# Optimization experiments

Measured on AMD Instinct MI355X. Metric: run time of the kernel, lower is better.

## Reference

```python
import jax, jax.numpy as jnp
import numpy as np

K, T, RHO, V, TH, EH, S, B = 50, 50, 300, 20000, 800, 200, 10, 256
DELTA = 0.005
LOG_DELTA = float(np.log(DELTA))
EPS = 1e-6


def setup_inputs() -> dict:
    key = jax.random.key(0)
    ks = jax.random.split(key, 32)
    f32 = jnp.float32
    rn = lambda i, shp, s=0.02: jax.random.normal(ks[i], shp, f32) * s
    inp = {
        "unique_tokens": jax.random.randint(ks[0], (100,), 0, V),
        "bows": jax.random.uniform(ks[1], (B, V), f32),
        "normalized_bows": jax.random.uniform(ks[2], (B, V), f32),
        "times": jax.random.randint(ks[3], (B,), 0, T),
        "sources": jax.random.randint(ks[4], (B,), 0, S),
        "rnn_inp": jax.random.normal(ks[5], (S, T, V), f32),
        "num_docs": 100000,
        # learned parameters
        "mu_q_alpha": rn(6, (K, T, RHO), 1.0),
        "logsigma_q_alpha": rn(7, (K, T, RHO), 0.1),
        "rho_W": rn(8, (V, RHO)),                 # Linear(rho_size -> vocab, no bias)
        "W1": rn(9, (TH, V + K)), "b1": jnp.zeros((TH,), f32),
        "W2": rn(10, (TH, TH)), "b2": jnp.zeros((TH,), f32),
        "mu_th_W": rn(11, (K, TH)), "mu_th_b": jnp.zeros((K,), f32),
        "ls_th_W": rn(12, (K, TH)), "ls_th_b": jnp.zeros((K,), f32),
        "eta_map_W": rn(13, (EH, V)), "eta_map_b": jnp.zeros((EH,), f32),
        "lstm_Wih": rn(14, (4 * EH, EH)), "lstm_Whh": rn(15, (4 * EH, EH)),
        "lstm_bih": jnp.zeros((4 * EH,), f32), "lstm_bhh": jnp.zeros((4 * EH,), f32),
        "mu_eta_W": rn(16, (K, EH + K)), "mu_eta_b": jnp.zeros((K,), f32),
        "ls_eta_W": rn(17, (K, EH + K)), "ls_eta_b": jnp.zeros((K,), f32),
        "cls_W": rn(18, (S, K)), "cls_b": jnp.zeros((S,), f32),
    }
    return inp


def _lstm(x_seq, Wih, Whh, bih, bhh):
    # x_seq: [T, S, EH]; torch gate order i,f,g,o
    def step(carry, x):
        h, c = carry
        z = x @ Wih.T + bih + h @ Whh.T + bhh
        i, f, g, o = jnp.split(z, 4, axis=-1)
        c = jax.nn.sigmoid(f) * c + jax.nn.sigmoid(i) * jnp.tanh(g)
        h = jax.nn.sigmoid(o) * jnp.tanh(c)
        return (h, c), h
    h0 = jnp.zeros((x_seq.shape[1], Whh.shape[1]), x_seq.dtype)
    _, out = jax.lax.scan(step, (h0, h0), x_seq)
    return out  # [T, S, EH]


def reference(unique_tokens, bows, normalized_bows, times, sources, rnn_inp, num_docs,
              mu_q_alpha, logsigma_q_alpha, rho_W, W1, b1, W2, b2,
              mu_th_W, mu_th_b, ls_th_W, ls_th_b, eta_map_W, eta_map_b,
              lstm_Wih, lstm_Whh, lstm_bih, lstm_bhh,
              mu_eta_W, mu_eta_b, ls_eta_W, ls_eta_b, cls_W, cls_b):
    # eval-mode semantics: reparameterize returns mu, dropout off
    bsz = bows.shape[0]
    coeff = num_docs / bsz

    # ---- alpha: eval-mode alphas_t == mu_q_alpha[:, t, :]; KL vectorized ----
    mu_a, ls_a = mu_q_alpha, logsigma_q_alpha  # [K, T, RHO]
    kl_a0 = 0.5 * jnp.sum((jnp.exp(ls_a[:, 0]) + mu_a[:, 0] ** 2) / (1.0 + EPS) - 1.0 - ls_a[:, 0])
    diff = mu_a[:, 1:] - mu_a[:, :-1]
    kl_at = 0.5 * jnp.sum((jnp.exp(ls_a[:, 1:]) + diff ** 2) / (DELTA + EPS) - 1.0 + LOG_DELTA - ls_a[:, 1:])
    kl_alpha = kl_a0 + kl_at
    alphas = jnp.transpose(mu_a, (1, 0, 2))  # [T, K, RHO]

    # ---- eta: LSTM over time (vmapped over sources as batch), then recurrence ----
    mapped = jnp.einsum('stv,hv->sth', rnn_inp, eta_map_W) + eta_map_b  # [S, T, EH]
    lstm_out = _lstm(jnp.transpose(mapped, (1, 0, 2)), lstm_Wih, lstm_Whh, lstm_bih, lstm_bhh)  # [T, S, EH]

    inp0 = jnp.concatenate([lstm_out[0], jnp.zeros((S, K), lstm_out.dtype)], axis=-1)
    mu0 = inp0 @ mu_eta_W.T + mu_eta_b
    ls0 = inp0 @ ls_eta_W.T + ls_eta_b  # no clipping at t=0 in original
    kl0 = 0.5 * jnp.sum((jnp.exp(ls0) + mu0 ** 2) / (1.0 + EPS) - 1.0 - ls0)

    def eta_step(carry, out_t):
        eta_prev, kl = carry
        inp_t = jnp.concatenate([out_t, eta_prev], axis=-1)
        mu_t = inp_t @ mu_eta_W.T + mu_eta_b
        ls_t = jnp.clip(inp_t @ ls_eta_W.T + ls_eta_b, -10.0, 10.0)
        kl_t = 0.5 * jnp.sum((jnp.exp(ls_t) + (mu_t - eta_prev) ** 2) / (DELTA + EPS) - 1.0 + LOG_DELTA - ls_t)
        return (mu_t, kl + kl_t), mu_t
    (_, kl_rest), etas_rest = jax.lax.scan(eta_step, (mu0, jnp.float32(0.0)), lstm_out[1:])
    etas = jnp.transpose(jnp.concatenate([mu0[None], etas_rest], axis=0), (1, 0, 2))  # [S, T, K]
    kl_eta = kl0 + kl_rest

    # ---- theta ----
    eta_std = etas[sources, times]  # [B, K]
    h = jax.nn.relu(jnp.concatenate([normalized_bows, eta_std], axis=1) @ W1.T + b1)
    h = jax.nn.relu(h @ W2.T + b2)
    mu_t = h @ mu_th_W.T + mu_th_b
    ls_t = jnp.clip(h @ ls_th_W.T + ls_th_b, -10.0, 10.0)
    theta = jax.nn.softmax(mu_t, axis=-1)
    kl_theta = (0.5 * jnp.sum((jnp.exp(ls_t) + (mu_t - eta_std) ** 2) / (1.0 + EPS) - 1.0 - ls_t)) * coeff

    # ---- beta and NLL ----
    logit = jnp.einsum('tkr,vr->tkv', alphas, rho_W)
    beta = jax.nn.softmax(logit, axis=-1)        # [T, K, V]
    beta_d = beta[times]                         # [B, K, V]
    loglik = jnp.log(jnp.einsum('bk,bkv->bv', theta, beta_d))
    nll = -jnp.sum(loglik * bows) * coeff

    # ---- source prediction loss (sum-reduced cross entropy) ----
    logits = theta @ cls_W.T + cls_b
    logp = jax.nn.log_softmax(logits, axis=-1)
    pred_loss = -jnp.sum(jnp.take_along_axis(logp, sources[:, None], axis=1)) * coeff

    nelbo = nll + kl_alpha + kl_eta + kl_theta + pred_loss
    return (nelbo, nll, kl_alpha, kl_eta, kl_theta, pred_loss)
```

## Files before the change

kernel.cpp:

```cpp
#include <hip/hip_runtime.h>

typedef unsigned int u32;
typedef unsigned short ushort_t;

#define NTOP 50
#define NT_T 50
#define NRHO 300
#define NVOC 20000
#define NTH 800
#define NEH 200
#define NSRC 10
#define NBAT 256

#define OFF_SCAL     0
#define OFF_MAPPED   16
#define OFF_HPRE     100016
#define OFF_H2       304816
#define OFF_Z        509616
#define OFF_DOCCNT   512120
#define OFF_DOCLIST  512176
#define MEMSET_BYTES ((size_t)524976 * 4)
#define OFF_XW       524976
#define OFF_BIAS2    924976
#define OFF_ETAS     925776
#define OFF_WCOEF    950776
#define OFF_W1E      963576
#define OFF_WHH_H    1003576
#define OFF_ETAWH    1083576
#define OFF_H1B      1096376
#define OFF_MAPB     1198776
#define OFF_WIHB     1256120
#define OFF_W2B      1356472
#define OFF_ALPHAB   1714872
#define OFF_RHOB     2124472
#define OFF_NBB      5339832
#define OFF_W1B      7899832
#define OFF_RNNB     16859832
#define OFF_EMWB     21979832
#define OFF_LOGITH   7899832

typedef _Float16 h2v __attribute__((ext_vector_type(2)));
typedef __bf16 bf16x8 __attribute__((ext_vector_type(8)));
typedef float f32x4 __attribute__((ext_vector_type(4)));

#define REP25(M) M(0) M(1) M(2) M(3) M(4) M(5) M(6) M(7) M(8) M(9) M(10) M(11) M(12) \
                 M(13) M(14) M(15) M(16) M(17) M(18) M(19) M(20) M(21) M(22) M(23) M(24)
#define REP7(M) M(0) M(1) M(2) M(3) M(4) M(5) M(6)

__device__ inline float dot2u(u32 a, u32 b, float c){
  h2v ha = __builtin_bit_cast(h2v, a), hb = __builtin_bit_cast(h2v, b);
#if __has_builtin(__builtin_amdgcn_fdot2)
  return __builtin_amdgcn_fdot2(ha, hb, c, false);
#else
  return c + (float)ha.x*(float)hb.x + (float)ha.y*(float)hb.y;
#endif
}

__device__ inline u32 packh2(float lo, float hi){
  h2v h; h.x = (_Float16)lo; h.y = (_Float16)hi;
  return __builtin_bit_cast(u32, h);
}

__device__ inline ushort_t f2bf(float f){
  u32 u = __builtin_bit_cast(u32, f);
  u = (u + 0x7FFFu + ((u >> 16) & 1u)) >> 16;
  return (ushort_t)u;
}

__device__ inline float fast_sig(float x){ return 1.f/(1.f + __expf(-x)); }
__device__ inline float fast_tanh(float x){ float e = __expf(2.f*x); return 1.f - 2.f/(e + 1.f); }

__device__ __forceinline__ void gl2lds16(const void* g, void* l){
  __builtin_amdgcn_global_load_lds((__attribute__((address_space(1))) void*)g,
                                   (__attribute__((address_space(3))) void*)l,
                                   16, 0, 0);
}

__device__ inline void blockReduceAdd(float v, float* red, float* target){
  int tid = threadIdx.x;
  red[tid] = v; __syncthreads();
  for (int o = blockDim.x >> 1; o > 0; o >>= 1){
    if (tid < o) red[tid] += red[tid + o];
    __syncthreads();
  }
  if (tid == 0) atomicAdd(target, red[0]);
}

__device__ inline void conv_seg(const float* __restrict__ src, int ldsrc,
                                int Mreal, int Kused,
                                ushort_t* __restrict__ dst, int Kp, int idx)
{
  int kb = Kp >> 3;
  int row = idx / kb, c = (idx - row*kb) << 3;
  ushort_t out[8];
  #pragma unroll
  for (int j = 0; j < 8; j++){
    float v = 0.f;
    int k = c + j;
    if (row < Mreal && k < Kused) v = src[(size_t)row*ldsrc + k];
    out[j] = f2bf(v);
  }
  *(uint4*)(dst + (size_t)row*Kp + c) = *(uint4*)out;
}

__global__ __launch_bounds__(256) void k_mega(
    const float* __restrict__ whh,
    const float* __restrict__ muEW, const float* __restrict__ lsEW,
    const float* __restrict__ bih, const float* __restrict__ bhh,
    const float* __restrict__ wih, const float* __restrict__ emapB,
    const float* __restrict__ W1, const int* __restrict__ times,
    const float* __restrict__ muq, const float* __restrict__ lsq,
    const float* __restrict__ rho, const float* __restrict__ nb,
    const float* __restrict__ rnn, const float* __restrict__ emapW,
    const float* __restrict__ W2f, float* __restrict__ W)
{
  int b = blockIdx.x, tid = threadIdx.x;
  __shared__ float red[256];
  if (b < 523){
    int idx = b*256 + tid;
    u32* whhH = (u32*)(W + OFF_WHH_H);
    u32* etaWH = (u32*)(W + OFF_ETAWH);
    if (idx < 80000){
      int j = idx/100; int i = idx - j*100;
      whhH[idx] = packh2(whh[j*200 + 2*i], whh[j*200 + 2*i + 1]);
    } else if (idx < 92800){
      int d = idx - 80000; int q = d >> 7; int i = d & 127;
      u32 v = 0u;
      if (i < 125){
        const float* src = (q < 50) ? (muEW + q*250) : (lsEW + (q-50)*250);
        v = packh2(src[2*i], src[2*i+1]);
      }
      etaWH[d] = v;
    } else if (idx < 93600){
      int j = idx - 92800;
      float acc = bih[j] + bhh[j];
      const float* wr = wih + (size_t)j*200;
      #pragma unroll 4
      for (int k = 0; k < 200; k++) acc += emapB[k]*wr[k];
      W[OFF_BIAS2 + j] = acc;
    } else if (idx < 133600){
      int d = idx - 93600; int j = d/50; int k = d - j*50;
      W[OFF_W1E + d] = W1[(size_t)j*20050 + 20000 + k];
    } else if (idx < 133856){
      int bb = idx - 133600; int t = times[bb];
      int* docCnt = (int*)(W + OFF_DOCCNT);
      int* docList = (int*)(W + OFF_DOCLIST);
      int pos = atomicAdd(&docCnt[t], 1);
      docList[t*256 + pos] = bb;
    }
  } else if (b < 923){
    int idx = (b-523)*256 + tid;
    int row = idx / 40, c = (idx - row*40) << 3;
    ushort_t out[8];
    const float* src = nullptr;
    if (row < 2500){ int t = row/50, k = row - t*50; src = muq + (size_t)k*15000 + t*300; }
    #pragma unroll
    for (int j = 0; j < 8; j++){
      int r = c + j;
      float v = (src && r < 300) ? src[r] : 0.f;
      out[j] = f2bf(v);
    }
    *(uint4*)((ushort_t*)(W + OFF_ALPHAB) + (size_t)row*320 + c) = *(uint4*)out;
  } else if (b < 4063){
    conv_seg(rho, 300, 20000, 300, (ushort_t*)(W + OFF_RHOB), 320, (b-923)*256 + tid);
  } else if (b < 6563){
    conv_seg(nb, 20000, 256, 20000, (ushort_t*)(W + OFF_NBB), 20000, (b-4063)*256 + tid);
  } else if (b < 15313){
    conv_seg(W1, 20050, 800, 20000, (ushort_t*)(W + OFF_W1B), 20000, (b-6563)*256 + tid);
  } else if (b < 20313){
    conv_seg(rnn, 20000, 500, 20000, (ushort_t*)(W + OFF_RNNB), 20000, (b-15313)*256 + tid);
  } else if (b < 22813){
    conv_seg(emapW, 20000, 200, 20000, (ushort_t*)(W + OFF_EMWB), 20000, (b-20313)*256 + tid);
  } else if (b < 22911){
    conv_seg(wih, 200, 800, 200, (ushort_t*)(W + OFF_WIHB), 224, (b-22813)*256 + tid);
  } else if (b < 23261){
    conv_seg(W2f, 800, 800, 800, (ushort_t*)(W + OFF_W2B), 800, (b-22911)*256 + tid);
  } else {
    const float inv_dl = 1.f/(0.005f + 1e-6f);
    const float logdl = -5.2983173665480363f;
    float local = 0.f;
    for (int idx = (b-23261)*256 + tid; idx < 750000; idx += 1024*256){
      int rem = idx % 15000; int t = rem / 300;
      float ls = lsq[idx]; float mu = muq[idx];
      if (t == 0){
        local += 0.5f*((__expf(ls) + mu*mu)/(1.f + 1e-6f) - 1.f - ls);
      } else {
        float d = mu - muq[idx - 300];
        local += 0.5f*((__expf(ls) + d*d)*inv_dl - 1.f + logdl - ls);
      }
    }
    blockReduceAdd(local, red, W + OFF_SCAL + 1);
  }
}

__global__ __launch_bounds__(256) void k_conv(const float* __restrict__ src, int ldsrc,
                                              int Mreal, int Kused,
                                              ushort_t* __restrict__ dst, int Mp, int Kp)
{
  int idx = blockIdx.x*256 + threadIdx.x;
  int kb = Kp >> 3;
  if (idx >= Mp*kb) return;
  conv_seg(src, ldsrc, Mreal, Kused, dst, Kp, idx);
}

template<int MODE>
__global__ __launch_bounds__(256) void mfma_nt(
    const ushort_t* __restrict__ A, int lda,
    const ushort_t* __restrict__ B, int ldb,
    float* __restrict__ C, _Float16* __restrict__ Ch, int ldc,
    const float* __restrict__ nBias,
    int M, int N, int mT, int kS, int chunks)
{
  __shared__ __align__(16) ushort_t As[128*32];
  __shared__ __align__(16) ushort_t Bs[128*32];
  int bid = blockIdx.x;
  int kIdx = bid % kS; int rest = bid / kS;
  int mIdx = rest % mT; int nIdx = rest / mT;
  int tid = threadIdx.x;
  int w = tid >> 6, l = tid & 63;
  int c0 = (int)(((long long)chunks * kIdx) / kS);
  int c1 = (int)(((long long)chunks * (kIdx+1)) / kS);
  int r0 = w*32;
  const ushort_t* ga0 = A + (size_t)(mIdx*128 + r0      + (l>>2))*lda + (l&3)*8;
  const ushort_t* ga1 = A + (size_t)(mIdx*128 + r0 + 16 + (l>>2))*lda + (l&3)*8;
  const ushort_t* gb0 = B + (size_t)(nIdx*128 + r0      + (l>>2))*ldb + (l&3)*8;
  const ushort_t* gb1 = B + (size_t)(nIdx*128 + r0 + 16 + (l>>2))*ldb + (l&3)*8;
  ushort_t* la = As + r0*32;
  ushort_t* lb = Bs + r0*32;
  int wr = (w >> 1)*64, wc = (w & 1)*64;
  int lr = l & 15, lq = l >> 4;
  f32x4 acc[4][4];
  #pragma unroll
  for (int i = 0; i < 4; i++)
    #pragma unroll
    for (int j = 0; j < 4; j++)
      acc[i][j] = (f32x4)0.f;

  for (int c = c0; c < c1; c++){
    size_t ko = (size_t)c * 32;
    gl2lds16(ga0 + ko, la);
    gl2lds16(ga1 + ko, la + 512);
    gl2lds16(gb0 + ko, lb);
    gl2lds16(gb1 + ko, lb + 512);
    __syncthreads();
    bf16x8 av[4], bv[4];
    #pragma unroll
    for (int i = 0; i < 4; i++)
      av[i] = *(const bf16x8*)(As + (wr + i*16 + lr)*32 + lq*8);
    #pragma unroll
    for (int j = 0; j < 4; j++)
      bv[j] = *(const bf16x8*)(Bs + (wc + j*16 + lr)*32 + lq*8);
    #pragma unroll
    for (int i = 0; i < 4; i++)
      #pragma unroll
      for (int j = 0; j < 4; j++)
        acc[i][j] = __builtin_amdgcn_mfma_f32_16x16x32_bf16(av[i], bv[j], acc[i][j], 0, 0, 0);
    __syncthreads();
  }
  if (MODE == 3){
    float* Z = C;
    #pragma unroll
    for (int i = 0; i < 4; i++){
      #pragma unroll
      for (int r = 0; r < 4; r++){
        int row = mIdx*128 + wr + i*16 + lq*4 + r;
        float p = 0.f;
        if (row < M){
          #pragma unroll
          for (int j = 0; j < 4; j++){
            int col = nIdx*128 + wc + j*16 + lr;
            if (col < N){
              float e = __expf(acc[i][j][r]);
              Ch[(size_t)row*ldc + col] = (_Float16)e;
              p += e;
            }
          }
        }
        p += __shfl_xor(p, 1, 16);
        p += __shfl_xor(p, 2, 16);
        p += __shfl_xor(p, 4, 16);
        p += __shfl_xor(p, 8, 16);
        if (lr == 0 && row < M) atomicAdd(&Z[row], p);
      }
    }
  } else {
    #pragma unroll
    for (int i = 0; i < 4; i++){
      #pragma unroll
      for (int r = 0; r < 4; r++){
        int row = mIdx*128 + wr + i*16 + lq*4 + r;
        if (row >= M) continue;
        #pragma unroll
        for (int j = 0; j < 4; j++){
          int col = nIdx*128 + wc + j*16 + lr;
          if (col >= N) continue;
          float v = acc[i][j][r];
          if (MODE == 0)      atomicAdd(&C[(size_t)row*ldc + col], v);
          else                C[(size_t)row*ldc + col] = v + nBias[col];
        }
      }
    }
  }
}

__global__ __launch_bounds__(512, 2) void k_lstm(
    const float* __restrict__ xw, const u32* __restrict__ whhH, const uint4* __restrict__ etaW4,
    const float* __restrict__ muEB, const float* __restrict__ lsEB,
    float* __restrict__ etas, float* __restrict__ W)
{
  int s = blockIdx.x; int tid = threadIdx.x;
  __shared__ uint4 hp4[2][32];
  __shared__ float zbuf[800];
  __shared__ float red[512];
  uint4 z4; z4.x = z4.y = z4.z = z4.w = 0u;
#define DECLW(i) uint4 wa##i = z4, wb##i = z4;
  REP25(DECLW)
#undef DECLW
  float ebias = 0.f;
  if (tid < 400){
    const uint4* ra = (const uint4*)(whhH + tid*100);
    const uint4* rb = (const uint4*)(whhH + (tid + 400)*100);
#define LDW(i) wa##i = ra[i]; wb##i = rb[i];
    REP25(LDW)
#undef LDW
  } else if (tid < 500){
    int q = tid - 400;
    const uint4* re = etaW4 + q*32;
#define LDA(i) wa##i = re[i];
    REP25(LDA)
#undef LDA
#define LDB(i) wb##i = re[25+i];
    REP7(LDB)
#undef LDB
    ebias = (q < 50) ? muEB[q] : lsEB[q - 50];
  }
  float creg = 0.f, muPrev = 0.f, klLocal = 0.f;
  if (tid < 64) ((uint4*)hp4)[tid] = z4;
  __syncthreads();
  const float inv_dl = 1.f/(0.005f + 1e-6f);
  const float logdl = -5.2983173665480363f;

  for (int t = 0; t < NT_T; t++){
    const uint4* hc = hp4[t & 1];
    uint4* hn = hp4[(t + 1) & 1];
    if (tid < 400){
      float a0=0.f,a1=0.f,a2=0.f,a3=0.f,b0=0.f,b1=0.f,b2=0.f,b3=0.f;
#define DOT(i) { uint4 h = hc[i]; \
      a0 = dot2u(wa##i.x, h.x, a0); a1 = dot2u(wa##i.y, h.y, a1); \
      a2 = dot2u(wa##i.z, h.z, a2); a3 = dot2u(wa##i.w, h.w, a3); \
      b0 = dot2u(wb##i.x, h.x, b0); b1 = dot2u(wb##i.y, h.y, b1); \
      b2 = dot2u(wb##i.z, h.z, b2); b3 = dot2u(wb##i.w, h.w, b3); }
      REP25(DOT)
#undef DOT
      const float* xr = xw + (size_t)(s*50 + t)*800;
      zbuf[tid]       = ((a0+a1)+(a2+a3)) + xr[tid];
      zbuf[tid + 400] = ((b0+b1)+(b2+b3)) + xr[tid + 400];
    }
    __syncthreads();
    if (tid < 200){
      float zi = zbuf[tid], zf = zbuf[200+tid], zg = zbuf[400+tid], zo = zbuf[600+tid];
      float ig = fast_sig(zi);
      float fg = fast_sig(zf);
      float gg = fast_tanh(zg);
      float og = fast_sig(zo);
      creg = fg*creg + ig*gg;
      float hv = og*fast_tanh(creg);
      ((_Float16*)hn)[tid] = (_Float16)hv;
    }
    __syncthreads();
    if (tid >= 400 && tid < 500){
      float e0 = ebias, e1 = 0.f, e2 = 0.f, e3 = 0.f;
#define DOTE(i) { uint4 h = hn[i]; \
      e0 = dot2u(wa##i.x, h.x, e0); e1 = dot2u(wa##i.y, h.y, e1); \
      e2 = dot2u(wa##i.z, h.z, e2); e3 = dot2u(wa##i.w, h.w, e3); }
      REP25(DOTE)
#undef DOTE
#define DOTP(i) { uint4 h = hc[25+i]; \
      e0 = dot2u(wb##i.x, h.x, e0); e1 = dot2u(wb##i.y, h.y, e1); \
      e2 = dot2u(wb##i.z, h.z, e2); e3 = dot2u(wb##i.w, h.w, e3); }
      REP7(DOTP)
#undef DOTP
      float eacc = (e0+e1)+(e2+e3);
      int q = tid - 400;
      if (q < 50){
        float mu = eacc;
        etas[(size_t)(s*50 + t)*50 + q] = mu;
        if (t == 0) klLocal += 0.5f*mu*mu/(1.f + 1e-6f);
        else { float d = mu - muPrev; klLocal += 0.5f*d*d*inv_dl; }
        muPrev = mu;
        ((_Float16*)hn)[200 + q] = (_Float16)mu;
      } else {
        float ls = eacc;
        if (t == 0) klLocal += 0.5f*(__expf(ls)/(1.f + 1e-6f) - 1.f - ls);
        else {
          ls = fminf(fmaxf(ls, -10.f), 10.f);
          klLocal += 0.5f*(__expf(ls)*inv_dl - 1.f + logdl - ls);
        }
      }
    }
  }
  __syncthreads();
  blockReduceAdd(klLocal, red, W + OFF_SCAL + 2);
}

__global__ __launch_bounds__(256) void k_h1(
    const float* __restrict__ hpre, const float* __restrict__ b1, const float* __restrict__ w1e,
    const float* __restrict__ etas, const int* __restrict__ times, const int* __restrict__ srcs,
    ushort_t* __restrict__ h1B)
{
  int b = blockIdx.x, tid = threadIdx.x;
  __shared__ float et[50];
  int tb = times[b], sb = srcs[b];
  if (tid < 50) et[tid] = etas[(size_t)(sb*50 + tb)*50 + tid];
  __syncthreads();
  for (int j = tid; j < 800; j += 256){
    float acc = hpre[(size_t)b*800 + j] + b1[j];
    const float* wrow = w1e + (size_t)j*50;
    #pragma unroll
    for (int k = 0; k < 50; k++) acc += et[k]*wrow[k];
    h1B[(size_t)b*800 + j] = f2bf(fmaxf(acc, 0.f));
  }
}

__global__ __launch_bounds__(256) void k_thfin(
    const float* __restrict__ h2g, const float* __restrict__ b2, const float* __restrict__ etas,
    const int* __restrict__ times, const int* __restrict__ srcs,
    const float* __restrict__ muW, const float* __restrict__ muB,
    const float* __restrict__ lsW, const float* __restrict__ lsB,
    const float* __restrict__ clsW, const float* __restrict__ clsB,
    const float* __restrict__ Zrow, float* __restrict__ wcoef, float* __restrict__ W)
{
  int b = blockIdx.x, tid = threadIdx.x;
  __shared__ float h2s[800], mu[50], lsv[50], et[50], th[50], lg[10], red[64], shm[2];
  for (int j = tid; j < 800; j += 256) h2s[j] = fmaxf(h2g[(size_t)b*800 + j] + b2[j], 0.f);
  int tb = times[b], sb = srcs[b];
  if (tid < 50) et[tid] = etas[(size_t)(sb*50 + tb)*50 + tid];
  __syncthreads();
  if (tid < 100){
    int q = (tid < 50) ? tid : tid - 50;
    const float* w = (tid < 50) ? (muW + (size_t)q*800) : (lsW + (size_t)q*800);
    float acc = (tid < 50) ? muB[q] : lsB[q];
    #pragma unroll 8
    for (int j = 0; j < 800; j++) acc += h2s[j]*w[j];
    if (tid < 50) mu[q] = acc;
    else lsv[q] = fminf(fmaxf(acc, -10.f), 10.f);
  }
  __syncthreads();
  if (tid == 0){ float m = -1e30f; for (int k = 0; k < 50; k++) m = fmaxf(m, mu[k]); shm[0] = m; }
  __syncthreads();
  if (tid < 50) th[tid] = __expf(mu[tid] - shm[0]);
  __syncthreads();
  if (tid == 0){ float z = 0.f; for (int k = 0; k < 50; k++) z += th[k]; shm[1] = z; }
  __syncthreads();
  if (tid < 64) red[tid] = 0.f;
  if (tid < 50){
    float t_ = th[tid]/shm[1]; th[tid] = t_;
    wcoef[(size_t)b*50 + tid] = t_/Zrow[tb*50 + tid];
    float d = mu[tid] - et[tid];
    red[tid] = 0.5f*((__expf(lsv[tid]) + d*d)/(1.f + 1e-6f) - 1.f - lsv[tid]);
  }
  __syncthreads();
  if (tid < 10){
    float a = clsB[tid];
    #pragma unroll
    for (int k = 0; k < 50; k++) a += th[k]*clsW[tid*50 + k];
    lg[tid] = a;
  }
  __syncthreads();
  if (tid == 0){
    float m = -1e30f; for (int i = 0; i < 10; i++) m = fmaxf(m, lg[i]);
    float z = 0.f; for (int i = 0; i < 10; i++) z += __expf(lg[i] - m);
    float lse = m + __logf(z);
    atomicAdd(W + OFF_SCAL + 4, lse - lg[sb]);
    float ssum = 0.f; for (int i = 0; i < 50; i++) ssum += red[i];
    atomicAdd(W + OFF_SCAL + 3, ssum);
  }
}

__global__ __launch_bounds__(256) void k_nll(
    const _Float16* __restrict__ E, const float* __restrict__ wcoef,
    const float* __restrict__ bows, float* __restrict__ W)
{
  int t = blockIdx.x/10, vc = blockIdx.x%10;
  int v0 = vc*2000;
  int tid = threadIdx.x;
  const int* docCnt = (const int*)(W + OFF_DOCCNT);
  const int* docList = (const int*)(W + OFF_DOCLIST);
  __shared__ float wch[64*50];
  __shared__ int ids[64];
  __shared__ float red[256];
  int nd = docCnt[t];
  float acc = 0.f;
  for (int d0 = 0; d0 < nd; d0 += 64){
    int ndc = min(64, nd - d0);
    __syncthreads();
    for (int i = tid; i < ndc*50; i += 256){
      int d = i/50, k = i - d*50;
      int bb = docList[t*256 + d0 + d];
      if (k == 0) ids[d] = bb;
      wch[i] = wcoef[(size_t)bb*50 + k];
    }
    __syncthreads();
    for (int v = v0 + tid; v < v0 + 2000; v += 256){
      float e[50];
      #pragma unroll
      for (int k = 0; k < 50; k++)
        e[k] = (float)E[(size_t)(t*50 + k)*NVOC + v];
      for (int d = 0; d < ndc; d++){
        float s = 0.f;
        #pragma unroll
        for (int k = 0; k < 50; k++) s += wch[d*50 + k]*e[k];
        acc += bows[(size_t)ids[d]*NVOC + v]*__logf(s);
      }
    }
  }
  __syncthreads();
  blockReduceAdd(acc, red, W + OFF_SCAL + 0);
}

__global__ void k_final(const float* __restrict__ W, const int* __restrict__ ndocs, float* __restrict__ out)
{
  if (blockIdx.x == 0 && threadIdx.x == 0){
    float coeff = (float)ndocs[0] / 256.f;
    const float* scal = W + OFF_SCAL;
    float nll  = -scal[0]*coeff;
    float kla  = scal[1];
    float kle  = scal[2];
    float klth = scal[3]*coeff;
    float pred = scal[4]*coeff;
    out[0] = nll + kla + kle + klth + pred;
    out[1] = nll; out[2] = kla; out[3] = kle; out[4] = klth; out[5] = pred;
  }
}

extern "C" void kernel_launch(void* const* d_in, const int* in_sizes, int n_in,
                              void* d_out, int out_size, void* d_ws, size_t ws_size,
                              hipStream_t stream)
{
  (void)in_sizes; (void)n_in; (void)out_size; (void)ws_size;
  const float* bows  = (const float*)d_in[1];
  const float* nb    = (const float*)d_in[2];
  const int*   times = (const int*)d_in[3];
  const int*   srcs  = (const int*)d_in[4];
  const float* rnn   = (const float*)d_in[5];
  const int*   ndocs = (const int*)d_in[6];
  const float* muq   = (const float*)d_in[7];
  const float* lsq   = (const float*)d_in[8];
  const float* rho   = (const float*)d_in[9];
  const float* W1    = (const float*)d_in[10];
  const float* b1    = (const float*)d_in[11];
  const float* W2    = (const float*)d_in[12];
  const float* b2    = (const float*)d_in[13];
  const float* muthW = (const float*)d_in[14];
  const float* muthB = (const float*)d_in[15];
  const float* lsthW = (const float*)d_in[16];
  const float* lsthB = (const float*)d_in[17];
  const float* emapW = (const float*)d_in[18];
  const float* emapB = (const float*)d_in[19];
  const float* wih   = (const float*)d_in[20];
  const float* whh   = (const float*)d_in[21];
  const float* bih   = (const float*)d_in[22];
  const float* bhh   = (const float*)d_in[23];
  const float* muEW  = (const float*)d_in[24];
  const float* muEB  = (const float*)d_in[25];
  const float* lsEW  = (const float*)d_in[26];
  const float* lsEB  = (const float*)d_in[27];
  const float* clsW  = (const float*)d_in[28];
  const float* clsB  = (const float*)d_in[29];

  float* W = (float*)d_ws;
  ushort_t* alphaB = (ushort_t*)(W + OFF_ALPHAB);
  ushort_t* rhoB   = (ushort_t*)(W + OFF_RHOB);
  ushort_t* nbB    = (ushort_t*)(W + OFF_NBB);
  ushort_t* w1B    = (ushort_t*)(W + OFF_W1B);
  ushort_t* rnnB   = (ushort_t*)(W + OFF_RNNB);
  ushort_t* emwB   = (ushort_t*)(W + OFF_EMWB);
  ushort_t* wihB   = (ushort_t*)(W + OFF_WIHB);
  ushort_t* w2B    = (ushort_t*)(W + OFF_W2B);
  ushort_t* mapB   = (ushort_t*)(W + OFF_MAPB);
  ushort_t* h1B    = (ushort_t*)(W + OFF_H1B);
  _Float16* Ehalf  = (_Float16*)(W + OFF_LOGITH);

  hipMemsetAsync(d_ws, 0, MEMSET_BYTES, stream);

  k_mega<<<24285, 256, 0, stream>>>(whh, muEW, lsEW, bih, bhh, wih, emapB, W1, times,
                                    muq, lsq, rho, nb, rnn, emapW, W2, W);

  mfma_nt<0><<<4*2*32, 256, 0, stream>>>(
      rnnB, 20000, emwB, 20000, W + OFF_MAPPED, nullptr, 200, nullptr,
      500, 200, 4, 32, 625);

  mfma_nt<0><<<2*7*20, 256, 0, stream>>>(
      nbB, 20000, w1B, 20000, W + OFF_HPRE, nullptr, 800, nullptr,
      256, 800, 2, 20, 625);

  mfma_nt<3><<<20*157, 256, 0, stream>>>(
      alphaB, 320, rhoB, 320, W + OFF_Z, Ehalf, 20000, nullptr,
      2500, 20000, 20, 1, 10);

  k_conv<<<56, 256, 0, stream>>>(W + OFF_MAPPED, 200, 500, 200, mapB, 512, 224);

  mfma_nt<2><<<4*7, 256, 0, stream>>>(
      mapB, 224, wihB, 224, W + OFF_XW, nullptr, 800, W + OFF_BIAS2,
      500, 800, 4, 1, 7);

  k_lstm<<<NSRC, 512, 0, stream>>>(W + OFF_XW, (const u32*)(W + OFF_WHH_H),
                                   (const uint4*)(W + OFF_ETAWH), muEB, lsEB,
                                   W + OFF_ETAS, W);

  k_h1<<<256, 256, 0, stream>>>(W + OFF_HPRE, b1, W + OFF_W1E, W + OFF_ETAS, times, srcs, h1B);

  mfma_nt<0><<<2*7*2, 256, 0, stream>>>(
      h1B, 800, w2B, 800, W + OFF_H2, nullptr, 800, nullptr,
      256, 800, 2, 2, 25);

  k_thfin<<<256, 256, 0, stream>>>(W + OFF_H2, b2, W + OFF_ETAS, times, srcs,
                                   muthW, muthB, lsthW, lsthB, clsW, clsB,
                                   W + OFF_Z, W + OFF_WCOEF, W);

  k_nll<<<500, 256, 0, stream>>>(Ehalf, W + OFF_WCOEF, bows, W);

  k_final<<<1, 64, 0, stream>>>(W, ndocs, (float*)d_out);
}
```

Baseline: 712.0 us.

## Fuse fp32-to-bf16 conversion into GEMM staging and drop separate conversion passes

Removes the large pre-pass that converted rnn_inp, bows, W1, emap, W2 and wih to bf16 copies in workspace. The GEMM kernel now loads fp32 directly and converts to bf16 while staging into padded shared memory. It also adds a dedicated logit/exp kernel that keeps A fragments in registers, writes E through an LDS tile with vector stores, and vectorises the NLL loop to handle two vocab entries per thread. This saves the extra read-write traffic of the conversion buffers, at the cost of fp32 global loads inside the GEMMs without the async LDS path.

```diff
diff --git a/kernel.cpp b/kernel.cpp
--- a/kernel.cpp
+++ b/kernel.cpp
@@ -27,17 +27,10 @@
 #define OFF_W1E      963576
 #define OFF_WHH_H    1003576
 #define OFF_ETAWH    1083576
-#define OFF_H1B      1096376
-#define OFF_MAPB     1198776
-#define OFF_WIHB     1256120
-#define OFF_W2B      1356472
-#define OFF_ALPHAB   1714872
-#define OFF_RHOB     2124472
-#define OFF_NBB      5339832
-#define OFF_W1B      7899832
-#define OFF_RNNB     16859832
-#define OFF_EMWB     21979832
-#define OFF_LOGITH   7899832
+#define OFF_H1       1096376
+#define OFF_ALPHAB   1301176
+#define OFF_RHOB     1710776
+#define OFF_LOGITH   4926136
 
 typedef _Float16 h2v __attribute__((ext_vector_type(2)));
 typedef __bf16 bf16x8 __attribute__((ext_vector_type(8)));
@@ -110,9 +103,7 @@
     const float* __restrict__ wih, const float* __restrict__ emapB,
     const float* __restrict__ W1, const int* __restrict__ times,
     const float* __restrict__ muq, const float* __restrict__ lsq,
-    const float* __restrict__ rho, const float* __restrict__ nb,
-    const float* __restrict__ rnn, const float* __restrict__ emapW,
-    const float* __restrict__ W2f, float* __restrict__ W)
+    const float* __restrict__ rho, float* __restrict__ W)
 {
   int b = blockIdx.x, tid = threadIdx.x;
   __shared__ float red[256];
@@ -163,23 +154,11 @@
     *(uint4*)((ushort_t*)(W + OFF_ALPHAB) + (size_t)row*320 + c) = *(uint4*)out;
   } else if (b < 4063){
     conv_seg(rho, 300, 20000, 300, (ushort_t*)(W + OFF_RHOB), 320, (b-923)*256 + tid);
-  } else if (b < 6563){
-    conv_seg(nb, 20000, 256, 20000, (ushort_t*)(W + OFF_NBB), 20000, (b-4063)*256 + tid);
-  } else if (b < 15313){
-    conv_seg(W1, 20050, 800, 20000, (ushort_t*)(W + OFF_W1B), 20000, (b-6563)*256 + tid);
-  } else if (b < 20313){
-    conv_seg(rnn, 20000, 500, 20000, (ushort_t*)(W + OFF_RNNB), 20000, (b-15313)*256 + tid);
-  } else if (b < 22813){
-    conv_seg(emapW, 20000, 200, 20000, (ushort_t*)(W + OFF_EMWB), 20000, (b-20313)*256 + tid);
-  } else if (b < 22911){
-    conv_seg(wih, 200, 800, 200, (ushort_t*)(W + OFF_WIHB), 224, (b-22813)*256 + tid);
-  } else if (b < 23261){
-    conv_seg(W2f, 800, 800, 800, (ushort_t*)(W + OFF_W2B), 800, (b-22911)*256 + tid);
   } else {
     const float inv_dl = 1.f/(0.005f + 1e-6f);
     const float logdl = -5.2983173665480363f;
     float local = 0.f;
-    for (int idx = (b-23261)*256 + tid; idx < 750000; idx += 1024*256){
+    for (int idx = (b-4063)*256 + tid; idx < 750000; idx += 1024*256){
       int rem = idx % 15000; int t = rem / 300;
       float ls = lsq[idx]; float mu = muq[idx];
       if (t == 0){
@@ -193,40 +172,53 @@
   }
 }
 
-__global__ __launch_bounds__(256) void k_conv(const float* __restrict__ src, int ldsrc,
-                                              int Mreal, int Kused,
-                                              ushort_t* __restrict__ dst, int Mp, int Kp)
-{
-  int idx = blockIdx.x*256 + threadIdx.x;
-  int kb = Kp >> 3;
-  if (idx >= Mp*kb) return;
-  conv_seg(src, ldsrc, Mreal, Kused, dst, Kp, idx);
-}
-
+__device__ __forceinline__ void stage_f32(
+    const float* __restrict__ src, int ld, int gRow, int rowMax,
+    int k0, int Kreal, ushort_t* __restrict__ dst)
+{
+  u32 pk[4];
+  const float* p = src + (size_t)gRow*ld + k0;
+  bool rowOK = gRow < rowMax;
+  if (rowOK && (k0 + 7 < Kreal)){
+    float2 f0 = *(const float2*)(p);
+    float2 f1 = *(const float2*)(p + 2);
+    float2 f2 = *(const float2*)(p + 4);
+    float2 f3 = *(const float2*)(p + 6);
+    pk[0] = (u32)f2bf(f0.x) | ((u32)f2bf(f0.y) << 16);
+    pk[1] = (u32)f2bf(f1.x) | ((u32)f2bf(f1.y) << 16);
+    pk[2] = (u32)f2bf(f2.x) | ((u32)f2bf(f2.y) << 16);
+    pk[3] = (u32)f2bf(f3.x) | ((u32)f2bf(f3.y) << 16);
+  } else {
+    #pragma unroll
+    for (int ii = 0; ii < 4; ii++){
+      int k = k0 + ii*2;
+      float x = (rowOK && k   < Kreal) ? p[ii*2]   : 0.f;
+      float y = (rowOK && k+1 < Kreal) ? p[ii*2+1] : 0.f;
+      pk[ii] = (u32)f2bf(x) | ((u32)f2bf(y) << 16);
+    }
+  }
+  *(uint4*)dst = *(uint4*)pk;
+}
+
+#define LDP 40
 template<int MODE>
-__global__ __launch_bounds__(256) void mfma_nt(
-    const ushort_t* __restrict__ A, int lda,
-    const ushort_t* __restrict__ B, int ldb,
-    float* __restrict__ C, _Float16* __restrict__ Ch, int ldc,
-    const float* __restrict__ nBias,
-    int M, int N, int mT, int kS, int chunks)
-{
-  __shared__ __align__(16) ushort_t As[128*32];
-  __shared__ __align__(16) ushort_t Bs[128*32];
+__global__ __launch_bounds__(256) void mfma_ntf(
+    const float* __restrict__ A, int lda,
+    const float* __restrict__ B, int ldb,
+    float* __restrict__ C, int ldc, const float* __restrict__ nBias,
+    int M, int N, int Kreal, int mT, int kS, int chunks)
+{
+  __shared__ __align__(16) ushort_t As[128*LDP];
+  __shared__ __align__(16) ushort_t Bs[128*LDP];
   int bid = blockIdx.x;
   int kIdx = bid % kS; int rest = bid / kS;
   int mIdx = rest % mT; int nIdx = rest / mT;
   int tid = threadIdx.x;
   int w = tid >> 6, l = tid & 63;
-  int c0 = (int)(((long long)chunks * kIdx) / kS);
-  int c1 = (int)(((long long)chunks * (kIdx+1)) / kS);
+  int c0 = (chunks * kIdx) / kS;
+  int c1 = (chunks * (kIdx+1)) / kS;
   int r0 = w*32;
-  const ushort_t* ga0 = A + (size_t)(mIdx*128 + r0      + (l>>2))*lda + (l&3)*8;
-  const ushort_t* ga1 = A + (size_t)(mIdx*128 + r0 + 16 + (l>>2))*lda + (l&3)*8;
-  const ushort_t* gb0 = B + (size_t)(nIdx*128 + r0      + (l>>2))*ldb + (l&3)*8;
-  const ushort_t* gb1 = B + (size_t)(nIdx*128 + r0 + 16 + (l>>2))*ldb + (l&3)*8;
-  ushort_t* la = As + r0*32;
-  ushort_t* lb = Bs + r0*32;
+  int row16 = l >> 2, kq = (l & 3) * 8;
   int wr = (w >> 1)*64, wc = (w & 1)*64;
   int lr = l & 15, lq = l >> 4;
   f32x4 acc[4][4];
@@ -237,19 +229,19 @@
       acc[i][j] = (f32x4)0.f;
 
   for (int c = c0; c < c1; c++){
-    size_t ko = (size_t)c * 32;
-    gl2lds16(ga0 + ko, la);
-    gl2lds16(ga1 + ko, la + 512);
-    gl2lds16(gb0 + ko, lb);
-    gl2lds16(gb1 + ko, lb + 512);
+    int k0 = c*32 + kq;
+    stage_f32(A, lda, mIdx*128 + r0 +      row16, M, k0, Kreal, As + (r0 +      row16)*LDP + kq);
+    stage_f32(A, lda, mIdx*128 + r0 + 16 + row16, M, k0, Kreal, As + (r0 + 16 + row16)*LDP + kq);
+    stage_f32(B, ldb, nIdx*128 + r0 +      row16, N, k0, Kreal, Bs + (r0 +      row16)*LDP + kq);
+    stage_f32(B, ldb, nIdx*128 + r0 + 16 + row16, N, k0, Kreal, Bs + (r0 + 16 + row16)*LDP + kq);
     __syncthreads();
     bf16x8 av[4], bv[4];
     #pragma unroll
     for (int i = 0; i < 4; i++)
-      av[i] = *(const bf16x8*)(As + (wr + i*16 + lr)*32 + lq*8);
+      av[i] = *(const bf16x8*)(As + (wr + i*16 + lr)*LDP + lq*8);
     #pragma unroll
     for (int j = 0; j < 4; j++)
-      bv[j] = *(const bf16x8*)(Bs + (wc + j*16 + lr)*32 + lq*8);
+      bv[j] = *(const bf16x8*)(Bs + (wc + j*16 + lr)*LDP + lq*8);
     #pragma unroll
     for (int i = 0; i < 4; i++)
       #pragma unroll
@@ -257,49 +249,121 @@
         acc[i][j] = __builtin_amdgcn_mfma_f32_16x16x32_bf16(av[i], bv[j], acc[i][j], 0, 0, 0);
     __syncthreads();
   }
-  if (MODE == 3){
-    float* Z = C;
-    #pragma unroll
-    for (int i = 0; i < 4; i++){
+  #pragma unroll
+  for (int i = 0; i < 4; i++){
+    #pragma unroll
+    for (int r = 0; r < 4; r++){
+      int row = mIdx*128 + wr + i*16 + lq*4 + r;
+      if (row >= M) continue;
       #pragma unroll
-      for (int r = 0; r < 4; r++){
-        int row = mIdx*128 + wr + i*16 + lq*4 + r;
-        float p = 0.f;
-        if (row < M){
+      for (int j = 0; j < 4; j++){
+        int col = nIdx*128 + wc + j*16 + lr;
+        if (col >= N) continue;
+        float v = acc[i][j][r];
+        if (MODE == 0) atomicAdd(&C[(size_t)row*ldc + col], v);
+        else           C[(size_t)row*ldc + col] = v + nBias[col];
+      }
+    }
+  }
+}
+
+__global__ __launch_bounds__(256) void mfma_e(
+    const ushort_t* __restrict__ A,
+    const ushort_t* __restrict__ B,
+    float* __restrict__ Z, _Float16* __restrict__ E)
+{
+  __shared__ __align__(16) ushort_t Bs[128*32];
+  __shared__ __align__(16) _Float16 Eb[64*136];
+  int bid = blockIdx.x;
+  int mIdx = bid % 20, nIdx = bid / 20;
+  int tid = threadIdx.x;
+  int w = tid >> 6, l = tid & 63;
+  int r0 = w*32;
+  const ushort_t* gb0 = B + (size_t)(nIdx*128 + r0      + (l>>2))*320 + (l&3)*8;
+  const ushort_t* gb1 = B + (size_t)(nIdx*128 + r0 + 16 + (l>>2))*320 + (l&3)*8;
+  ushort_t* lb = Bs + r0*32;
+  int wr = (w >> 1)*64, wc = (w & 1)*64;
+  int lr = l & 15, lq = l >> 4;
+  int aRow[4];
+  #pragma unroll
+  for (int i = 0; i < 4; i++) aRow[i] = mIdx*128 + wr + i*16 + lr;
+  f32x4 acc[4][4];
+  #pragma unroll
+  for (int i = 0; i < 4; i++)
+    #pragma unroll
+    for (int j = 0; j < 4; j++)
+      acc[i][j] = (f32x4)0.f;
+
+  bf16x8 avn[4];
+  #pragma unroll
+  for (int i = 0; i < 4; i++)
+    avn[i] = *(const bf16x8*)(A + (size_t)aRow[i]*320 + lq*8);
+
+  for (int c = 0; c < 10; c++){
+    gl2lds16(gb0 + c*32, lb);
+    gl2lds16(gb1 + c*32, lb + 512);
+    bf16x8 av[4];
+    #pragma unroll
+    for (int i = 0; i < 4; i++) av[i] = avn[i];
+    if (c < 9){
+      #pragma unroll
+      for (int i = 0; i < 4; i++)
+        avn[i] = *(const bf16x8*)(A + (size_t)aRow[i]*320 + (c+1)*32 + lq*8);
+    }
+    __syncthreads();
+    bf16x8 bv[4];
+    #pragma unroll
+    for (int j = 0; j < 4; j++)
+      bv[j] = *(const bf16x8*)(Bs + (wc + j*16 + lr)*32 + lq*8);
+    #pragma unroll
+    for (int i = 0; i < 4; i++)
+      #pragma unroll
+      for (int j = 0; j < 4; j++)
+        acc[i][j] = __builtin_amdgcn_mfma_f32_16x16x32_bf16(av[i], bv[j], acc[i][j], 0, 0, 0);
+    __syncthreads();
+  }
+  int half = w >> 1;
+  for (int h = 0; h < 2; h++){
+    if (half == h){
+      #pragma unroll
+      for (int i = 0; i < 4; i++){
+        #pragma unroll
+        for (int r = 0; r < 4; r++){
+          int lrow = i*16 + lq*4 + r;
+          int grow = mIdx*128 + h*64 + lrow;
+          float p = 0.f;
           #pragma unroll
           for (int j = 0; j < 4; j++){
             int col = nIdx*128 + wc + j*16 + lr;
-            if (col < N){
-              float e = __expf(acc[i][j][r]);
-              Ch[(size_t)row*ldc + col] = (_Float16)e;
-              p += e;
-            }
+            float e = (col < NVOC) ? __expf(acc[i][j][r]) : 0.f;
+            Eb[lrow*136 + wc + j*16 + lr] = (_Float16)e;
+            p += e;
           }
+          p += __shfl_xor(p, 1, 16);
+          p += __shfl_xor(p, 2, 16);
+          p += __shfl_xor(p, 4, 16);
+          p += __shfl_xor(p, 8, 16);
+          if (lr == 0 && grow < 2500) atomicAdd(&Z[grow], p);
         }
-        p += __shfl_xor(p, 1, 16);
-        p += __shfl_xor(p, 2, 16);
-        p += __shfl_xor(p, 4, 16);
-        p += __shfl_xor(p, 8, 16);
-        if (lr == 0 && row < M) atomicAdd(&Z[row], p);
-      }
-    }
-  } else {
-    #pragma unroll
-    for (int i = 0; i < 4; i++){
-      #pragma unroll
-      for (int r = 0; r < 4; r++){
-        int row = mIdx*128 + wr + i*16 + lq*4 + r;
-        if (row >= M) continue;
+      }
+    }
+    __syncthreads();
+    int lrow = tid >> 2, coff = (tid & 3) * 32;
+    int grow = mIdx*128 + h*64 + lrow;
+    if (grow < 2500){
+      int gcol0 = nIdx*128 + coff;
+      if (gcol0 + 31 < NVOC){
         #pragma unroll
-        for (int j = 0; j < 4; j++){
-          int col = nIdx*128 + wc + j*16 + lr;
-          if (col >= N) continue;
-          float v = acc[i][j][r];
-          if (MODE == 0)      atomicAdd(&C[(size_t)row*ldc + col], v);
-          else                C[(size_t)row*ldc + col] = v + nBias[col];
+        for (int cc = 0; cc < 4; cc++)
+          *(uint4*)(E + (size_t)grow*NVOC + gcol0 + cc*8) = *(uint4*)(Eb + lrow*136 + coff + cc*8);
+      } else {
+        for (int cc = 0; cc < 32; cc++){
+          int gc = gcol0 + cc;
+          if (gc < NVOC) E[(size_t)grow*NVOC + gc] = Eb[lrow*136 + coff + cc];
         }
       }
     }
+    __syncthreads();
   }
 }
 
@@ -406,7 +470,7 @@
 __global__ __launch_bounds__(256) void k_h1(
     const float* __restrict__ hpre, const float* __restrict__ b1, const float* __restrict__ w1e,
     const float* __restrict__ etas, const int* __restrict__ times, const int* __restrict__ srcs,
-    ushort_t* __restrict__ h1B)
+    float* __restrict__ h1)
 {
   int b = blockIdx.x, tid = threadIdx.x;
   __shared__ float et[50];
@@ -418,7 +482,7 @@
     const float* wrow = w1e + (size_t)j*50;
     #pragma unroll
     for (int k = 0; k < 50; k++) acc += et[k]*wrow[k];
-    h1B[(size_t)b*800 + j] = f2bf(fmaxf(acc, 0.f));
+    h1[(size_t)b*800 + j] = fmaxf(acc, 0.f);
   }
 }
 
@@ -501,16 +565,23 @@
       wch[i] = wcoef[(size_t)bb*50 + k];
     }
     __syncthreads();
-    for (int v = v0 + tid; v < v0 + 2000; v += 256){
-      float e[50];
+    for (int v = v0 + tid*2; v < v0 + 2000; v += 512){
+      float ex[50], ey[50];
       #pragma unroll
-      for (int k = 0; k < 50; k++)
-        e[k] = (float)E[(size_t)(t*50 + k)*NVOC + v];
+      for (int k = 0; k < 50; k++){
+        u32 pk = *(const u32*)(E + (size_t)(t*50 + k)*NVOC + v);
+        h2v h = __builtin_bit_cast(h2v, pk);
+        ex[k] = (float)h.x; ey[k] = (float)h.y;
+      }
       for (int d = 0; d < ndc; d++){
-        float s = 0.f;
+        float sx = 0.f, sy = 0.f;
         #pragma unroll
-        for (int k = 0; k < 50; k++) s += wch[d*50 + k]*e[k];
-        acc += bows[(size_t)ids[d]*NVOC + v]*__logf(s);
+        for (int k = 0; k < 50; k++){
+          float wv = wch[d*50 + k];
+          sx += wv*ex[k]; sy += wv*ey[k];
+        }
+        float2 bw = *(const float2*)(bows + (size_t)ids[d]*NVOC + v);
+        acc += bw.x*__logf(sx) + bw.y*__logf(sy);
       }
     }
   }
@@ -571,48 +642,37 @@
   float* W = (float*)d_ws;
   ushort_t* alphaB = (ushort_t*)(W + OFF_ALPHAB);
   ushort_t* rhoB   = (ushort_t*)(W + OFF_RHOB);
-  ushort_t* nbB    = (ushort_t*)(W + OFF_NBB);
-  ushort_t* w1B    = (ushort_t*)(W + OFF_W1B);
-  ushort_t* rnnB   = (ushort_t*)(W + OFF_RNNB);
-  ushort_t* emwB   = (ushort_t*)(W + OFF_EMWB);
-  ushort_t* wihB   = (ushort_t*)(W + OFF_WIHB);
-  ushort_t* w2B    = (ushort_t*)(W + OFF_W2B);
-  ushort_t* mapB   = (ushort_t*)(W + OFF_MAPB);
-  ushort_t* h1B    = (ushort_t*)(W + OFF_H1B);
   _Float16* Ehalf  = (_Float16*)(W + OFF_LOGITH);
 
   hipMemsetAsync(d_ws, 0, MEMSET_BYTES, stream);
 
-  k_mega<<<24285, 256, 0, stream>>>(whh, muEW, lsEW, bih, bhh, wih, emapB, W1, times,
-                                    muq, lsq, rho, nb, rnn, emapW, W2, W);
-
-  mfma_nt<0><<<4*2*32, 256, 0, stream>>>(
-      rnnB, 20000, emwB, 20000, W + OFF_MAPPED, nullptr, 200, nullptr,
-      500, 200, 4, 32, 625);
-
-  mfma_nt<0><<<2*7*20, 256, 0, stream>>>(
-      nbB, 20000, w1B, 20000, W + OFF_HPRE, nullptr, 800, nullptr,
-      256, 800, 2, 20, 625);
-
-  mfma_nt<3><<<20*157, 256, 0, stream>>>(
-      alphaB, 320, rhoB, 320, W + OFF_Z, Ehalf, 20000, nullptr,
-      2500, 20000, 20, 1, 10);
-
-  k_conv<<<56, 256, 0, stream>>>(W + OFF_MAPPED, 200, 500, 200, mapB, 512, 224);
-
-  mfma_nt<2><<<4*7, 256, 0, stream>>>(
-      mapB, 224, wihB, 224, W + OFF_XW, nullptr, 800, W + OFF_BIAS2,
-      500, 800, 4, 1, 7);
+  k_mega<<<5087, 256, 0, stream>>>(whh, muEW, lsEW, bih, bhh, wih, emapB, W1, times,
+                                   muq, lsq, rho, W);
+
+  mfma_e<<<20*157, 256, 0, stream>>>(alphaB, rhoB, W + OFF_Z, Ehalf);
+
+  mfma_ntf<0><<<4*2*32, 256, 0, stream>>>(
+      rnn, 20000, emapW, 20000, W + OFF_MAPPED, 200, nullptr,
+      500, 200, 20000, 4, 32, 625);
+
+  mfma_ntf<2><<<4*7, 256, 0, stream>>>(
+      W + OFF_MAPPED, 200, wih, 200, W + OFF_XW, 800, W + OFF_BIAS2,
+      500, 800, 200, 4, 1, 7);
 
   k_lstm<<<NSRC, 512, 0, stream>>>(W + OFF_XW, (const u32*)(W + OFF_WHH_H),
                                    (const uint4*)(W + OFF_ETAWH), muEB, lsEB,
                                    W + OFF_ETAS, W);
 
-  k_h1<<<256, 256, 0, stream>>>(W + OFF_HPRE, b1, W + OFF_W1E, W + OFF_ETAS, times, srcs, h1B);
-
-  mfma_nt<0><<<2*7*2, 256, 0, stream>>>(
-      h1B, 800, w2B, 800, W + OFF_H2, nullptr, 800, nullptr,
-      256, 800, 2, 2, 25);
+  mfma_ntf<0><<<2*7*20, 256, 0, stream>>>(
+      nb, 20000, W1, 20050, W + OFF_HPRE, 800, nullptr,
+      256, 800, 20000, 2, 20, 625);
+
+  k_h1<<<256, 256, 0, stream>>>(W + OFF_HPRE, b1, W + OFF_W1E, W + OFF_ETAS, times, srcs,
+                                W + OFF_H1);
+
+  mfma_ntf<0><<<2*7*2, 256, 0, stream>>>(
+      W + OFF_H1, 800, W2, 800, W + OFF_H2, 800, nullptr,
+      256, 800, 800, 2, 2, 25);
 
   k_thfin<<<256, 256, 0, stream>>>(W + OFF_H2, b2, W + OFF_ETAS, times, srcs,
                                    muthW, muthB, lsthW, lsthB, clsW, clsB,
```

Result: slower. 810.9 us (+13.9%).
